# Kernel optimization log

Measured on AMD Instinct MI355X. Metric: run time of the kernel, lower is better.

The kernel has to match this reference:

```python
import jax, jax.numpy as jnp
import numpy as np

N, DIM, G, K = 100000, 512, 4, 16
GD = DIM // G
EPS = 1e-5

def _ln(x, g, b):
    mu = jnp.mean(x, axis=-1, keepdims=True)
    var = jnp.mean((x - mu) ** 2, axis=-1, keepdims=True)
    return (x - mu) / jnp.sqrt(var + EPS) * g + b

def setup_inputs() -> dict:
    key = jax.random.key(0)
    ks = jax.random.split(key, 12)
    s = 1.0 / np.sqrt(GD)
    return {
        "features": jax.random.normal(ks[0], (N, DIM), jnp.float32),
        "coords": jax.random.uniform(ks[1], (N, 3), jnp.float32),
        "neighbors": jax.random.randint(ks[2], (N, K), 0, N),
        "Wq": jax.random.normal(ks[3], (G, GD, GD), jnp.float32) * s,
        "Wk": jax.random.normal(ks[4], (G, GD, GD), jnp.float32) * s,
        "Wv": jax.random.normal(ks[5], (G, GD, GD), jnp.float32) * s,
        "Wo": jax.random.normal(ks[6], (DIM, DIM), jnp.float32) / np.sqrt(DIM),
        "bo": jnp.zeros((DIM,), jnp.float32),
        "ln1_g": jnp.ones((DIM,), jnp.float32),
        "ln1_b": jnp.zeros((DIM,), jnp.float32),
        "ln2_g": jnp.ones((DIM,), jnp.float32),
        "ln2_b": jnp.zeros((DIM,), jnp.float32),
        "W1": jax.random.normal(ks[7], (2 * DIM, DIM), jnp.float32) / np.sqrt(DIM),
        "b1": jnp.zeros((2 * DIM,), jnp.float32),
        "W2": jax.random.normal(ks[8], (DIM, 2 * DIM), jnp.float32) / np.sqrt(2 * DIM),
        "b2": jnp.zeros((DIM,), jnp.float32),
    }

def reference(features, coords, neighbors, Wq, Wk, Wv, Wo, bo, ln1_g, ln1_b, ln2_g, ln2_b, W1, b1, W2, b2):
    n = features.shape[0]
    residual = features
    x = _ln(features, ln1_g, ln1_b)
    xg = x.reshape(n, G, GD)                      # chunk along feature dim == group reshape
    # per-group Linear (no bias): y = x @ W.T with W (out,in)
    q = jnp.einsum('ngd,god->ngo', xg, Wq)
    k = jnp.einsum('ngd,god->ngo', xg, Wk)
    v = jnp.einsum('ngd,god->ngo', xg, Wv)
    nk = k[neighbors]                             # (N,K,G,GD) gather
    nv = v[neighbors]
    scale = jnp.asarray(1.0 / np.sqrt(GD), x.dtype)
    scores = jnp.einsum('ngd,nkgd->nkg', q, nk) * scale
    w = jax.nn.softmax(scores, axis=1)
    attn = jnp.einsum('nkg,nkgd->ngd', w, nv).reshape(n, DIM)
    out = attn @ Wo.T + bo + residual
    res2 = out
    y = _ln(out, ln2_g, ln2_b)
    y = jax.nn.gelu(y @ W1.T + b1, approximate=False) @ W2.T + b2
    return y + res2
```

## Files before the change

### kernel.cpp

```cpp
#include <hip/hip_runtime.h>
#include <hip/hip_bf16.h>
#include <math.h>

#define NPTS 100000
#define PAD_ROWS 100096
#define DIM 512
#define GRP 4
#define GD 128
#define K_NBR 16
#define EPS 1e-5f

using bf16x8 = __attribute__((ext_vector_type(8))) short;
using f32x4  = __attribute__((ext_vector_type(4))) float;
using short4v = __attribute__((ext_vector_type(4))) short;

__device__ inline float bf2f(short s) {
    unsigned u = ((unsigned)(unsigned short)s) << 16;
    union { unsigned u; float f; } c; c.u = u; return c.f;
}
__device__ inline short f2bf(float f) {
    union { float f; unsigned u; } c; c.f = f;
    unsigned u = c.u;
    unsigned r = (u + 0x7fffu + ((u >> 16) & 1u)) >> 16;
    return (short)r;
}

__device__ __forceinline__ void gload_lds16(short* lds, const short* g) {
    __builtin_amdgcn_global_load_lds(
        (const __attribute__((address_space(1))) unsigned int*)g,
        (__attribute__((address_space(3))) unsigned int*)lds, 16, 0, 0);
}

__global__ void cvt_kernel(const float* __restrict__ src, short* __restrict__ dst, int n) {
    int i = blockIdx.x * blockDim.x + threadIdx.x;
    int stride = gridDim.x * blockDim.x;
    for (; i < n; i += stride) dst[i] = f2bf(src[i]);
}

__global__ void prep_m_kernel(const float* __restrict__ wq, const float* __restrict__ wk,
                              short* __restrict__ mt) {
    int ge = blockIdx.x;
    int g = ge >> 7, e = ge & 127;
    int d = threadIdx.x;
    const float* Wq = wq + (size_t)g * GD * GD;
    const float* Wk = wk + (size_t)g * GD * GD;
    float acc = 0.0f;
    for (int o = 0; o < GD; ++o)
        acc += Wq[(size_t)o * GD + d] * Wk[(size_t)o * GD + e];
    mt[(size_t)ge * GD + d] = f2bf(acc * 0.08838834764831845f);
}

__global__ void prep_wov_kernel(const float* __restrict__ wo, const float* __restrict__ wv,
                                short* __restrict__ wov) {
    int o = blockIdx.x;
    int i = threadIdx.x;
    int g = i >> 7, i0 = i & 127;
    float acc = 0.0f;
    for (int d = 0; d < GD; ++d)
        acc += wo[(size_t)o * DIM + g * GD + d] * wv[((size_t)g * GD + d) * GD + i0];
    wov[(size_t)o * DIM + i] = f2bf(acc);
}

__global__ void ln_kernel(const float* __restrict__ in, const float* __restrict__ g,
                          const float* __restrict__ b, short* __restrict__ out) {
    int row = blockIdx.x;
    int tid = threadIdx.x;
    if (row >= NPTS) {
        short4v z; z[0] = 0; z[1] = 0; z[2] = 0; z[3] = 0;
        *(short4v*)(out + (size_t)row * DIM + tid * 4) = z;
        return;
    }
    const float4 x = *(const float4*)(in + (size_t)row * DIM + tid * 4);
    float s  = x.x + x.y + x.z + x.w;
    float sq = x.x * x.x + x.y * x.y + x.z * x.z + x.w * x.w;
    for (int m = 1; m < 64; m <<= 1) {
        s  += __shfl_xor(s, m);
        sq += __shfl_xor(sq, m);
    }
    __shared__ float ss[2], ssq[2];
    int wv = tid >> 6;
    if ((tid & 63) == 0) { ss[wv] = s; ssq[wv] = sq; }
    __syncthreads();
    s = ss[0] + ss[1]; sq = ssq[0] + ssq[1];
    float mu = s * (1.0f / DIM);
    float var = sq * (1.0f / DIM) - mu * mu;
    float rstd = rsqrtf(var + EPS);
    const float4 gg = *(const float4*)(g + tid * 4);
    const float4 bb = *(const float4*)(b + tid * 4);
    short4v o;
    o[0] = f2bf((x.x - mu) * rstd * gg.x + bb.x);
    o[1] = f2bf((x.y - mu) * rstd * gg.y + bb.y);
    o[2] = f2bf((x.z - mu) * rstd * gg.z + bb.z);
    o[3] = f2bf((x.w - mu) * rstd * gg.w + bb.w);
    *(short4v*)(out + (size_t)row * DIM + tid * 4) = o;
}

template<int NK>
__device__ __forceinline__ void gemm_tile(
        const short* __restrict__ aBase, int as_,
        const short* __restrict__ bBase, int bs_,
        short* As, short* Bs, f32x4 (&acc)[4][4]) {
    int tid = threadIdx.x;
    int lane = tid & 63, wave = tid >> 6;
    int wr = wave >> 1, wc = wave & 1;
    int r = lane & 15, ks = lane >> 4;
    int ldRow = tid >> 2;
    int ldCol = (tid & 3) * 8;
    for (int kt = 0; kt < NK; ++kt) {
        __syncthreads();
        const short* aS = aBase + kt * 32;
        const short* bS = bBase + kt * 32;
        gload_lds16(As + (ldRow)      * 32 + ldCol, aS + (size_t)(ldRow)      * as_ + ldCol);
        gload_lds16(As + (ldRow + 64) * 32 + ldCol, aS + (size_t)(ldRow + 64) * as_ + ldCol);
        gload_lds16(Bs + (ldRow)      * 32 + ldCol, bS + (size_t)(ldRow)      * bs_ + ldCol);
        gload_lds16(Bs + (ldRow + 64) * 32 + ldCol, bS + (size_t)(ldRow + 64) * bs_ + ldCol);
        __syncthreads();
        bf16x8 a[4];
        #pragma unroll
        for (int m = 0; m < 4; ++m)
            a[m] = *(const bf16x8*)(As + (wr * 64 + m * 16 + r) * 32 + ks * 8);
        #pragma unroll
        for (int n = 0; n < 4; ++n) {
            bf16x8 b = *(const bf16x8*)(Bs + (wc * 64 + n * 16 + r) * 32 + ks * 8);
            #pragma unroll
            for (int m = 0; m < 4; ++m)
                acc[m][n] = __builtin_amdgcn_mfma_f32_16x16x32_bf16(a[m], b, acc[m][n], 0, 0, 0);
        }
    }
}

__global__ __launch_bounds__(256) void qproj_kernel(
        const short* __restrict__ x, const short* __restrict__ mt,
        short* __restrict__ qp) {
    __shared__ short As[128 * 32], Bs[128 * 32];
    int nwg = gridDim.x;
    int bid = blockIdx.x;
    int tile = (bid & 7) * (nwg >> 3) + (bid >> 3);
    int rb = tile >> 2, g = tile & 3;
    int rowbase = rb * 128;
    int tid = threadIdx.x;
    int lane = tid & 63, wave = tid >> 6;
    int wr = wave >> 1, wc = wave & 1;
    int r = lane & 15, ks = lane >> 4;
    f32x4 acc[4][4];
    #pragma unroll
    for (int m = 0; m < 4; ++m)
        #pragma unroll
        for (int n = 0; n < 4; ++n)
            #pragma unroll
            for (int e = 0; e < 4; ++e) acc[m][n][e] = 0.0f;
    gemm_tile<4>(x + (size_t)rowbase * DIM + g * GD, DIM,
                 mt + (size_t)g * GD * GD, GD, As, Bs, acc);
    #pragma unroll
    for (int m = 0; m < 4; ++m)
        #pragma unroll
        for (int n = 0; n < 4; ++n)
            #pragma unroll
            for (int rr = 0; rr < 4; ++rr) {
                int orow = rowbase + wr * 64 + m * 16 + ks * 4 + rr;
                int lcol = wc * 64 + n * 16 + r;
                qp[(size_t)orow * DIM + g * GD + lcol] = f2bf(acc[m][n][rr]);
            }
}

__global__ __launch_bounds__(256) void attn_kernel(
        const short* __restrict__ qp, const short* __restrict__ x,
        const int* __restrict__ nbrs, short* __restrict__ t_out) {
    int b = blockIdx.x;
    int xcd = b & 7;
    int g = xcd >> 1;
    int quad = (b >> 3) * 2 + (xcd & 1);
    int tid = threadIdx.x;
    int wv = tid >> 6, lane = tid & 63;
    int n = quad * 4 + wv;
    int s = lane >> 4, t = lane & 15;
    int4 nbj = *(const int4*)(nbrs + (size_t)n * K_NBR + s * 4);
    int nbarr[4] = {nbj.x, nbj.y, nbj.z, nbj.w};
    size_t goff = (size_t)g * GD + t * 8;
    size_t qbase = (size_t)n * DIM + goff;
    bf16x8 qf = *(const bf16x8*)(qp + qbase);
    float qv[8];
    #pragma unroll
    for (int e = 0; e < 8; ++e) qv[e] = bf2f(qf[e]);
    bf16x8 xf[4];
    #pragma unroll
    for (int p = 0; p < 4; ++p)
        xf[p] = *(const bf16x8*)(x + (size_t)nbarr[p] * DIM + goff);
    float sc[4];
    #pragma unroll
    for (int p = 0; p < 4; ++p) {
        float dd = 0.0f;
        #pragma unroll
        for (int e = 0; e < 8; ++e) dd += qv[e] * bf2f(xf[p][e]);
        dd += __shfl_xor(dd, 1);
        dd += __shfl_xor(dd, 2);
        dd += __shfl_xor(dd, 4);
        dd += __shfl_xor(dd, 8);
        sc[p] = dd;
    }
    float mx = fmaxf(fmaxf(sc[0], sc[1]), fmaxf(sc[2], sc[3]));
    mx = fmaxf(mx, __shfl_xor(mx, 16));
    mx = fmaxf(mx, __shfl_xor(mx, 32));
    float ew[4]; float ssum = 0.0f;
    #pragma unroll
    for (int p = 0; p < 4; ++p) { ew[p] = __expf(sc[p] - mx); ssum += ew[p]; }
    ssum += __shfl_xor(ssum, 16);
    ssum += __shfl_xor(ssum, 32);
    float acc[8];
    #pragma unroll
    for (int d0 = 0; d0 < 8; ++d0) acc[d0] = 0.0f;
    #pragma unroll
    for (int p = 0; p < 4; ++p) {
        #pragma unroll
        for (int d0 = 0; d0 < 8; ++d0) acc[d0] += ew[p] * bf2f(xf[p][d0]);
    }
    #pragma unroll
    for (int d0 = 0; d0 < 8; ++d0) {
        acc[d0] += __shfl_xor(acc[d0], 16);
        acc[d0] += __shfl_xor(acc[d0], 32);
    }
    if (s == 0) {
        float inv = 1.0f / ssum;
        bf16x8 o;
        #pragma unroll
        for (int d0 = 0; d0 < 8; ++d0) o[d0] = f2bf(acc[d0] * inv);
        *(bf16x8*)(t_out + qbase) = o;
    }
}

__global__ __launch_bounds__(256) void outproj_kernel(
        const short* __restrict__ tbuf, const short* __restrict__ wov,
        const float* __restrict__ bo, const float* __restrict__ features,
        float* __restrict__ out) {
    __shared__ short As[128 * 32], Bs[128 * 32];
    int nwg = gridDim.x;
    int bid = blockIdx.x;
    int tile = (bid & 7) * (nwg >> 3) + (bid >> 3);
    int rb = tile >> 2, cb = tile & 3;
    int rowbase = rb * 128, colbase = cb * 128;
    int tid = threadIdx.x;
    int lane = tid & 63, wave = tid >> 6;
    int wr = wave >> 1, wc = wave & 1;
    int r = lane & 15, ks = lane >> 4;
    f32x4 acc[4][4];
    #pragma unroll
    for (int m = 0; m < 4; ++m)
        #pragma unroll
        for (int n = 0; n < 4; ++n)
            #pragma unroll
            for (int e = 0; e < 4; ++e) acc[m][n][e] = 0.0f;
    gemm_tile<16>(tbuf + (size_t)rowbase * DIM, DIM,
                  wov + (size_t)colbase * DIM, DIM, As, Bs, acc);
    #pragma unroll
    for (int m = 0; m < 4; ++m)
        #pragma unroll
        for (int n = 0; n < 4; ++n)
            #pragma unroll
            for (int rr = 0; rr < 4; ++rr) {
                int orow = rowbase + wr * 64 + m * 16 + ks * 4 + rr;
                int ocol = colbase + wc * 64 + n * 16 + r;
                if (orow < NPTS) {
                    out[(size_t)orow * DIM + ocol] =
                        acc[m][n][rr] + bo[ocol] + features[(size_t)orow * DIM + ocol];
                }
            }
}

__global__ __launch_bounds__(256) void ffn1_kernel(
        const short* __restrict__ y, const short* __restrict__ w1,
        const float* __restrict__ b1, short* __restrict__ h) {
    __shared__ short As[128 * 32], Bs[128 * 32];
    int nwg = gridDim.x;
    int bid = blockIdx.x;
    int tile = (bid & 7) * (nwg >> 3) + (bid >> 3);
    int rb = tile >> 3, cb = tile & 7;
    int rowbase = rb * 128, colbase = cb * 128;
    int tid = threadIdx.x;
    int lane = tid & 63, wave = tid >> 6;
    int wr = wave >> 1, wc = wave & 1;
    int r = lane & 15, ks = lane >> 4;
    f32x4 acc[4][4];
    #pragma unroll
    for (int m = 0; m < 4; ++m)
        #pragma unroll
        for (int n = 0; n < 4; ++n)
            #pragma unroll
            for (int e = 0; e < 4; ++e) acc[m][n][e] = 0.0f;
    gemm_tile<16>(y + (size_t)rowbase * DIM, DIM,
                  w1 + (size_t)colbase * DIM, DIM, As, Bs, acc);
    #pragma unroll
    for (int m = 0; m < 4; ++m)
        #pragma unroll
        for (int n = 0; n < 4; ++n)
            #pragma unroll
            for (int rr = 0; rr < 4; ++rr) {
                int orow = rowbase + wr * 64 + m * 16 + ks * 4 + rr;
                int ocol = colbase + wc * 64 + n * 16 + r;
                float xv = acc[m][n][rr] + b1[ocol];
                float xc = fminf(fmaxf(xv, -9.0f), 9.0f);
                float u = xc * (0.7978845608028654f + 0.0356774081f * xc * xc);
                float e2 = __expf(2.0f * u);
                float th = (e2 - 1.0f) / (e2 + 1.0f);
                float gl = 0.5f * xv * (1.0f + th);
                h[(size_t)orow * (2 * DIM) + ocol] = f2bf(gl);
            }
}

__global__ __launch_bounds__(256) void ffn2_kernel(
        const short* __restrict__ h, const short* __restrict__ w2,
        const float* __restrict__ b2, float* __restrict__ out) {
    __shared__ short As[128 * 32], Bs[128 * 32];
    int nwg = gridDim.x;
    int bid = blockIdx.x;
    int tile = (bid & 7) * (nwg >> 3) + (bid >> 3);
    int rb = tile >> 2, cb = tile & 3;
    int rowbase = rb * 128, colbase = cb * 128;
    int tid = threadIdx.x;
    int lane = tid & 63, wave = tid >> 6;
    int wr = wave >> 1, wc = wave & 1;
    int r = lane & 15, ks = lane >> 4;
    f32x4 acc[4][4];
    #pragma unroll
    for (int m = 0; m < 4; ++m)
        #pragma unroll
        for (int n = 0; n < 4; ++n)
            #pragma unroll
            for (int e = 0; e < 4; ++e) acc[m][n][e] = 0.0f;
    gemm_tile<32>(h + (size_t)rowbase * (2 * DIM), 2 * DIM,
                  w2 + (size_t)colbase * (2 * DIM), 2 * DIM, As, Bs, acc);
    #pragma unroll
    for (int m = 0; m < 4; ++m)
        #pragma unroll
        for (int n = 0; n < 4; ++n)
            #pragma unroll
            for (int rr = 0; rr < 4; ++rr) {
                int orow = rowbase + wr * 64 + m * 16 + ks * 4 + rr;
                int ocol = colbase + wc * 64 + n * 16 + r;
                if (orow < NPTS) {
                    size_t idx = (size_t)orow * DIM + ocol;
                    out[idx] = acc[m][n][rr] + b2[ocol] + out[idx];
                }
            }
}

extern "C" void kernel_launch(void* const* d_in, const int* in_sizes, int n_in,
                              void* d_out, int out_size, void* d_ws, size_t ws_size,
                              hipStream_t stream) {
    const float* features = (const float*)d_in[0];
    const int*   neighbors = (const int*)d_in[2];
    const float* Wq = (const float*)d_in[3];
    const float* Wk = (const float*)d_in[4];
    const float* Wv = (const float*)d_in[5];
    const float* Wo = (const float*)d_in[6];
    const float* bo = (const float*)d_in[7];
    const float* ln1_g = (const float*)d_in[8];
    const float* ln1_b = (const float*)d_in[9];
    const float* ln2_g = (const float*)d_in[10];
    const float* ln2_b = (const float*)d_in[11];
    const float* W1 = (const float*)d_in[12];
    const float* b1 = (const float*)d_in[13];
    const float* W2 = (const float*)d_in[14];
    const float* b2 = (const float*)d_in[15];
    float* out = (float*)d_out;

    size_t slotElems = (size_t)PAD_ROWS * DIM;
    short* s0 = (short*)d_ws;
    short* s1 = s0 + slotElems;
    short* s2 = s1 + slotElems;
    short* mt_b  = s2 + slotElems;
    short* wov_b = mt_b + GRP * GD * GD;
    short* w1_b  = wov_b + DIM * DIM;
    short* w2_b  = w1_b + 2 * DIM * DIM;

    cvt_kernel<<<256, 256, 0, stream>>>(W1, w1_b, 2 * DIM * DIM);
    cvt_kernel<<<256, 256, 0, stream>>>(W2, w2_b, 2 * DIM * DIM);
    prep_m_kernel<<<GRP * GD, GD, 0, stream>>>(Wq, Wk, mt_b);
    prep_wov_kernel<<<DIM, DIM, 0, stream>>>(Wo, Wv, wov_b);

    ln_kernel<<<PAD_ROWS, 128, 0, stream>>>(features, ln1_g, ln1_b, s0);

    qproj_kernel<<<(PAD_ROWS / 128) * 4, 256, 0, stream>>>(s0, mt_b, s1);

    attn_kernel<<<NPTS, 256, 0, stream>>>(s1, s0, neighbors, s2);

    outproj_kernel<<<(PAD_ROWS / 128) * 4, 256, 0, stream>>>(s2, wov_b, bo, features, out);

    ln_kernel<<<PAD_ROWS, 128, 0, stream>>>(out, ln2_g, ln2_b, s0);

    ffn1_kernel<<<(PAD_ROWS / 128) * 8, 256, 0, stream>>>(s0, w1_b, b1, s1);

    ffn2_kernel<<<(PAD_ROWS / 128) * 4, 256, 0, stream>>>(s1, w2_b, b2, out);
}
```

Measured before the change: 1.164 ms.

## Double-buffer LDS tiles in shared GEMM loop to overlap loads with MFMA

Splits the GEMM k-loop into staging and compute helpers and adds a second pair of LDS buffers. The next k-slice is staged into the alternate buffer while MFMAs run on the current one, and the loop is unrolled by two. The aim is to hide global-to-LDS load latency and drop one barrier per k-step in the q-projection, output-projection and both FFN GEMMs. LDS use per block doubles to 32 KB, which may lower occupancy.

After: 1.125 ms. -3.4%, faster.

```diff
diff --git a/kernel.cpp b/kernel.cpp
--- a/kernel.cpp
+++ b/kernel.cpp
@@ -95,44 +95,62 @@
     *(short4v*)(out + (size_t)row * DIM + tid * 4) = o;
 }
 
+__device__ __forceinline__ void stage_tile(short* As, short* Bs,
+        const short* aS, int as_, const short* bS, int bs_, int tid) {
+    int ldRow = tid >> 2;
+    int ldCol = (tid & 3) * 8;
+    gload_lds16(As + (ldRow)      * 32 + ldCol, aS + (size_t)(ldRow)      * as_ + ldCol);
+    gload_lds16(As + (ldRow + 64) * 32 + ldCol, aS + (size_t)(ldRow + 64) * as_ + ldCol);
+    gload_lds16(Bs + (ldRow)      * 32 + ldCol, bS + (size_t)(ldRow)      * bs_ + ldCol);
+    gload_lds16(Bs + (ldRow + 64) * 32 + ldCol, bS + (size_t)(ldRow + 64) * bs_ + ldCol);
+}
+
+__device__ __forceinline__ void compute_tile(const short* As, const short* Bs,
+        int wr, int wc, int r, int ks, f32x4 (&acc)[4][4]) {
+    bf16x8 a[4];
+    #pragma unroll
+    for (int m = 0; m < 4; ++m)
+        a[m] = *(const bf16x8*)(As + (wr * 64 + m * 16 + r) * 32 + ks * 8);
+    #pragma unroll
+    for (int n = 0; n < 4; ++n) {
+        bf16x8 b = *(const bf16x8*)(Bs + (wc * 64 + n * 16 + r) * 32 + ks * 8);
+        #pragma unroll
+        for (int m = 0; m < 4; ++m)
+            acc[m][n] = __builtin_amdgcn_mfma_f32_16x16x32_bf16(a[m], b, acc[m][n], 0, 0, 0);
+    }
+}
+
 template<int NK>
 __device__ __forceinline__ void gemm_tile(
         const short* __restrict__ aBase, int as_,
         const short* __restrict__ bBase, int bs_,
-        short* As, short* Bs, f32x4 (&acc)[4][4]) {
+        short* As0, short* Bs0, short* As1, short* Bs1, f32x4 (&acc)[4][4]) {
     int tid = threadIdx.x;
     int lane = tid & 63, wave = tid >> 6;
     int wr = wave >> 1, wc = wave & 1;
     int r = lane & 15, ks = lane >> 4;
-    int ldRow = tid >> 2;
-    int ldCol = (tid & 3) * 8;
-    for (int kt = 0; kt < NK; ++kt) {
+    stage_tile(As0, Bs0, aBase, as_, bBase, bs_, tid);
+    __syncthreads();
+    #pragma unroll
+    for (int kt = 0; kt < NK; kt += 2) {
+        if (kt + 1 < NK)
+            stage_tile(As1, Bs1, aBase + (kt + 1) * 32, as_, bBase + (kt + 1) * 32, bs_, tid);
+        compute_tile(As0, Bs0, wr, wc, r, ks, acc);
         __syncthreads();
-        const short* aS = aBase + kt * 32;
-        const short* bS = bBase + kt * 32;
-        gload_lds16(As + (ldRow)      * 32 + ldCol, aS + (size_t)(ldRow)      * as_ + ldCol);
-        gload_lds16(As + (ldRow + 64) * 32 + ldCol, aS + (size_t)(ldRow + 64) * as_ + ldCol);
-        gload_lds16(Bs + (ldRow)      * 32 + ldCol, bS + (size_t)(ldRow)      * bs_ + ldCol);
-        gload_lds16(Bs + (ldRow + 64) * 32 + ldCol, bS + (size_t)(ldRow + 64) * bs_ + ldCol);
+        if (kt + 2 < NK)
+            stage_tile(As0, Bs0, aBase + (kt + 2) * 32, as_, bBase + (kt + 2) * 32, bs_, tid);
+        compute_tile(As1, Bs1, wr, wc, r, ks, acc);
         __syncthreads();
-        bf16x8 a[4];
-        #pragma unroll
-        for (int m = 0; m < 4; ++m)
-            a[m] = *(const bf16x8*)(As + (wr * 64 + m * 16 + r) * 32 + ks * 8);
-        #pragma unroll
-        for (int n = 0; n < 4; ++n) {
-            bf16x8 b = *(const bf16x8*)(Bs + (wc * 64 + n * 16 + r) * 32 + ks * 8);
-            #pragma unroll
-            for (int m = 0; m < 4; ++m)
-                acc[m][n] = __builtin_amdgcn_mfma_f32_16x16x32_bf16(a[m], b, acc[m][n], 0, 0, 0);
-        }
-    }
-}
+    }
+}
+
+#define GEMM_LDS \
+    __shared__ short As0[128 * 32], Bs0[128 * 32], As1[128 * 32], Bs1[128 * 32]
 
 __global__ __launch_bounds__(256) void qproj_kernel(
         const short* __restrict__ x, const short* __restrict__ mt,
         short* __restrict__ qp) {
-    __shared__ short As[128 * 32], Bs[128 * 32];
+    GEMM_LDS;
     int nwg = gridDim.x;
     int bid = blockIdx.x;
     int tile = (bid & 7) * (nwg >> 3) + (bid >> 3);
@@ -150,7 +168,7 @@
             #pragma unroll
             for (int e = 0; e < 4; ++e) acc[m][n][e] = 0.0f;
     gemm_tile<4>(x + (size_t)rowbase * DIM + g * GD, DIM,
-                 mt + (size_t)g * GD * GD, GD, As, Bs, acc);
+                 mt + (size_t)g * GD * GD, GD, As0, Bs0, As1, Bs1, acc);
     #pragma unroll
     for (int m = 0; m < 4; ++m)
         #pragma unroll
@@ -232,7 +250,7 @@
         const short* __restrict__ tbuf, const short* __restrict__ wov,
         const float* __restrict__ bo, const float* __restrict__ features,
         float* __restrict__ out) {
-    __shared__ short As[128 * 32], Bs[128 * 32];
+    GEMM_LDS;
     int nwg = gridDim.x;
     int bid = blockIdx.x;
     int tile = (bid & 7) * (nwg >> 3) + (bid >> 3);
@@ -250,7 +268,7 @@
             #pragma unroll
             for (int e = 0; e < 4; ++e) acc[m][n][e] = 0.0f;
     gemm_tile<16>(tbuf + (size_t)rowbase * DIM, DIM,
-                  wov + (size_t)colbase * DIM, DIM, As, Bs, acc);
+                  wov + (size_t)colbase * DIM, DIM, As0, Bs0, As1, Bs1, acc);
     #pragma unroll
     for (int m = 0; m < 4; ++m)
         #pragma unroll
@@ -269,7 +287,7 @@
 __global__ __launch_bounds__(256) void ffn1_kernel(
         const short* __restrict__ y, const short* __restrict__ w1,
         const float* __restrict__ b1, short* __restrict__ h) {
-    __shared__ short As[128 * 32], Bs[128 * 32];
+    GEMM_LDS;
     int nwg = gridDim.x;
     int bid = blockIdx.x;
     int tile = (bid & 7) * (nwg >> 3) + (bid >> 3);
@@ -287,7 +305,7 @@
             #pragma unroll
             for (int e = 0; e < 4; ++e) acc[m][n][e] = 0.0f;
     gemm_tile<16>(y + (size_t)rowbase * DIM, DIM,
-                  w1 + (size_t)colbase * DIM, DIM, As, Bs, acc);
+                  w1 + (size_t)colbase * DIM, DIM, As0, Bs0, As1, Bs1, acc);
     #pragma unroll
     for (int m = 0; m < 4; ++m)
         #pragma unroll
@@ -309,7 +327,7 @@
 __global__ __launch_bounds__(256) void ffn2_kernel(
         const short* __restrict__ h, const short* __restrict__ w2,
         const float* __restrict__ b2, float* __restrict__ out) {
-    __shared__ short As[128 * 32], Bs[128 * 32];
+    GEMM_LDS;
     int nwg = gridDim.x;
     int bid = blockIdx.x;
     int tile = (bid & 7) * (nwg >> 3) + (bid >> 3);
@@ -327,7 +345,7 @@
             #pragma unroll
             for (int e = 0; e < 4; ++e) acc[m][n][e] = 0.0f;
     gemm_tile<32>(h + (size_t)rowbase * (2 * DIM), 2 * DIM,
-                  w2 + (size_t)colbase * (2 * DIM), 2 * DIM, As, Bs, acc);
+                  w2 + (size_t)colbase * (2 * DIM), 2 * DIM, As0, Bs0, As1, Bs1, acc);
     #pragma unroll
     for (int m = 0; m < 4; ++m)
         #pragma unroll
```
